# Kernel tuning notes

Hardware: AMD Instinct MI355X
Metric: run time of the kernel (lower is better)

The kernel has to match this reference:

```python
import jax, jax.numpy as jnp
import numpy as np

C = 128
N0, N1, N2 = 1000000, 100000, 10000


def setup_inputs() -> dict:
    key = jax.random.key(0)
    ks = jax.random.split(key, 9)
    return {
        "x0": jax.random.normal(ks[0], (N0, C), dtype=jnp.float32),
        "x1": jax.random.normal(ks[1], (N1, C), dtype=jnp.float32),
        "x2": jax.random.normal(ks[2], (N2, C), dtype=jnp.float32),
        "cluster1": jax.random.randint(ks[3], (N0,), 0, N1, dtype=jnp.int32),
        "cluster2": jax.random.randint(ks[4], (N1,), 0, N2, dtype=jnp.int32),
        "Wf2c0": jax.random.normal(ks[5], (C, C), dtype=jnp.float32) / np.sqrt(C),
        "Wf2c1": jax.random.normal(ks[6], (C, C), dtype=jnp.float32) / np.sqrt(C),
        "Wc2f0": jax.random.normal(ks[7], (C, C), dtype=jnp.float32) / np.sqrt(C),
        "Wc2f1": jax.random.normal(ks[8], (C, C), dtype=jnp.float32) / np.sqrt(C),
    }


def _segment_mean(x, idx, num_segments):
    # scatter-mean: sum per cluster / count (count clamped to 1 -> empty clusters give 0)
    s = jax.ops.segment_sum(x, idx, num_segments=num_segments)
    cnt = jax.ops.segment_sum(jnp.ones((x.shape[0], 1), x.dtype), idx, num_segments=num_segments)
    return s / jnp.maximum(cnt, 1.0)


def reference(x0, x1, x2, cluster1, cluster2, Wf2c0, Wf2c1, Wc2f0, Wc2f1):
    n1, n2 = x1.shape[0], x2.shape[0]
    # scale 0: x0 + gather(coarse_to_fine_0(x1), cluster1)
    y0 = x0 + (x1 @ Wc2f0.T)[cluster1]
    # scale 1: x1 + fine_to_coarse_0(scatter_mean(x0, cluster1)) + gather(coarse_to_fine_1(x2), cluster2)
    y1 = x1 + _segment_mean(x0, cluster1, n1) @ Wf2c0.T + (x2 @ Wc2f1.T)[cluster2]
    # scale 2: x2 + fine_to_coarse_1(scatter_mean(x1, cluster2))
    y2 = x2 + _segment_mean(x1, cluster2, n2) @ Wf2c1.T
    return (y0, y1, y2)
```

## Files before the change

kernel.cpp:

```cpp
#include <hip/hip_runtime.h>

#define C128 128
#define WSTRIDE 136

typedef __attribute__((ext_vector_type(2))) float f32x2;
typedef __attribute__((ext_vector_type(4))) float f32x4;
typedef __attribute__((ext_vector_type(8))) short short8;

__device__ __forceinline__ short f2bf(float f) {
  union { float f; unsigned u; } v; v.f = f;
  unsigned r = (v.u + 0x7fffu + ((v.u >> 16) & 1u)) >> 16;
  return (short)r;
}

__device__ __forceinline__ void stage_W(const float* __restrict__ W, ushort* Wl) {
  const int tid = threadIdx.x;
#pragma unroll
  for (int c = 0; c < 16; ++c) {
    const int e = (c * 256 + tid) * 4;
    const int row = e >> 7, col = e & 127;
    f32x4 v = *(const f32x4*)(W + e);
    ushort4 u;
    u.x = (ushort)f2bf(v.x); u.y = (ushort)f2bf(v.y);
    u.z = (ushort)f2bf(v.z); u.w = (ushort)f2bf(v.w);
    *(ushort4*)(Wl + row * WSTRIDE + col) = u;
  }
}

__device__ __forceinline__ void gemm_body(
    const float* __restrict__ A, const ushort* __restrict__ Wl,
    const float* __restrict__ add,
    const int* __restrict__ gidx, const float* __restrict__ gtab,
    float* __restrict__ out, int R, int blockrow)
{
  const int tid  = threadIdx.x;
  const int wave = tid >> 6;
  const int lane = tid & 63;
  const int r16  = lane & 15;
  const int kg   = lane >> 4;

  const int rowbase = blockrow + wave * 16;
  if (rowbase >= R) return;
  const int arow_i  = rowbase + r16;
  const int lrow    = arow_i < R ? arow_i : (R - 1);

  f32x4 acc[8];
#pragma unroll
  for (int i = 0; i < 8; ++i) acc[i] = (f32x4){0.f, 0.f, 0.f, 0.f};

  const float* arow = A + (long long)lrow * C128;

#pragma unroll
  for (int ks = 0; ks < 4; ++ks) {
    const int k0 = ks * 32 + kg * 8;
    f32x4 alo = *(const f32x4*)(arow + k0);
    f32x4 ahi = *(const f32x4*)(arow + k0 + 4);
    short8 af;
    af[0] = f2bf(alo.x); af[1] = f2bf(alo.y);
    af[2] = f2bf(alo.z); af[3] = f2bf(alo.w);
    af[4] = f2bf(ahi.x); af[5] = f2bf(ahi.y);
    af[6] = f2bf(ahi.z); af[7] = f2bf(ahi.w);
#pragma unroll
    for (int nf = 0; nf < 8; ++nf) {
      short8 bf = *(const short8*)(Wl + (nf * 16 + r16) * WSTRIDE + k0);
      acc[nf] = __builtin_amdgcn_mfma_f32_16x16x32_bf16(af, bf, acc[nf], 0, 0, 0);
    }
  }

#pragma unroll
  for (int i = 0; i < 4; ++i) {
    const int orow = rowbase + kg * 4 + i;
    if (orow >= R) continue;
    const float* addrow = add ? add + (long long)orow * C128 : nullptr;
    const float* grow = gidx ? gtab + (long long)gidx[orow] * C128 : nullptr;
    float* orow_p = out + (long long)orow * C128;
#pragma unroll
    for (int nf = 0; nf < 8; ++nf) {
      const int oc = nf * 16 + r16;
      float v = acc[nf][i];
      if (addrow) v += addrow[oc];
      if (grow)   v += grow[oc];
      orow_p[oc] = v;
    }
  }
}

__global__ __launch_bounds__(256) void pre_gemm(
    const float* __restrict__ x1, const float* __restrict__ W1, float* __restrict__ t1, int n1,
    const float* __restrict__ x2, const float* __restrict__ W2, float* __restrict__ t2, int n2,
    int* __restrict__ zbuf, int zlen, int B1)
{
  __shared__ ushort Wl[C128 * WSTRIDE];
  {
    const int nb  = gridDim.x;
    const int per = (zlen + nb - 1) / nb;
    const int zs  = blockIdx.x * per;
    const int ze  = (zs + per < zlen) ? zs + per : zlen;
    for (int k = zs + threadIdx.x; k < ze; k += 256) zbuf[k] = 0;
  }
  if ((int)blockIdx.x < B1) {
    stage_W(W1, Wl); __syncthreads();
    gemm_body(x1, Wl, nullptr, nullptr, nullptr, t1, n1, blockIdx.x * 64);
  } else {
    stage_W(W2, Wl); __syncthreads();
    gemm_body(x2, Wl, nullptr, nullptr, nullptr, t2, n2, (blockIdx.x - B1) * 64);
  }
}

__global__ __launch_bounds__(256) void post_gemm(
    const float* __restrict__ mean0, const float* __restrict__ Wa,
    const float* __restrict__ x1, const int* __restrict__ cluster2,
    const float* __restrict__ t2, float* __restrict__ y1, int n1,
    const float* __restrict__ mean1, const float* __restrict__ Wb,
    const float* __restrict__ x2, float* __restrict__ y2, int n2, int B1)
{
  __shared__ ushort Wl[C128 * WSTRIDE];
  if ((int)blockIdx.x < B1) {
    stage_W(Wa, Wl); __syncthreads();
    gemm_body(mean0, Wl, x1, cluster2, t2, y1, n1, blockIdx.x * 64);
  } else {
    stage_W(Wb, Wl); __syncthreads();
    gemm_body(mean1, Wl, x2, nullptr, nullptr, y2, n2, (blockIdx.x - B1) * 64);
  }
}

__global__ __launch_bounds__(256) void hist2(
    const int* __restrict__ cl1, int n0, int* __restrict__ cnt0,
    const int* __restrict__ cl2, int n1, int* __restrict__ cnt1)
{
  int i = blockIdx.x * blockDim.x + threadIdx.x;
  const int stride = gridDim.x * blockDim.x;
  const int total = n0 + n1;
  for (; i < total; i += stride) {
    if (i < n0) atomicAdd(&cnt0[cl1[i]], 1);
    else        atomicAdd(&cnt1[cl2[i - n0]], 1);
  }
}

__global__ __launch_bounds__(256) void scan2(
    const int* __restrict__ cnt0, int* __restrict__ off0, int* __restrict__ cur0, int n1,
    const int* __restrict__ cnt1, int* __restrict__ off1, int* __restrict__ cur1, int n2,
    int* __restrict__ tot)
{
  const int p1 = (n1 + 255) & ~255;
  const int i  = blockIdx.x * blockDim.x + threadIdx.x;
  const int lane = threadIdx.x & 63;

  const int* cnt; int* off; int* cur; int* t; int j; int nn;
  if (i < p1) { cnt = cnt0; off = off0; cur = cur0; t = tot + 0; j = i;      nn = n1; }
  else        { cnt = cnt1; off = off1; cur = cur1; t = tot + 1; j = i - p1; nn = n2; }

  int c = (j < nn) ? cnt[j] : 0;
  int pref = c;
#pragma unroll
  for (int d = 1; d < 64; d <<= 1) {
    int v = __shfl_up(pref, d);
    if (lane >= d) pref += v;
  }
  const int wave_total = __shfl(pref, 63);
  int base = 0;
  if (lane == 63) base = atomicAdd(t, wave_total);
  base = __shfl(base, 63);

  if (j < nn) {
    const int o = base + (pref - c);
    off[j] = o;
    cur[j] = o;
  }
}

__global__ __launch_bounds__(256) void fill2(
    const int* __restrict__ cl1, int n0, int* __restrict__ cur0, int* __restrict__ idx0,
    const int* __restrict__ cl2, int n1, int* __restrict__ cur1, int* __restrict__ idx1)
{
  int i = blockIdx.x * blockDim.x + threadIdx.x;
  const int stride = gridDim.x * blockDim.x;
  const int total = n0 + n1;
  for (; i < total; i += stride) {
    if (i < n0) { int p = atomicAdd(&cur0[cl1[i]], 1); idx0[p] = i; }
    else        { int k = i - n0; int p = atomicAdd(&cur1[cl2[k]], 1); idx1[p] = k; }
  }
}

__device__ __forceinline__ void cr_one(
    int wid, int lane, const float* __restrict__ x,
    const int* __restrict__ idxp, const int* __restrict__ offp,
    const int* __restrict__ cntp, const float* __restrict__ trow,
    float* __restrict__ yb, float* __restrict__ meanp)
{
  const int n = cntp[wid];
  const int o = offp[wid];

  f32x2 tc = {0.f, 0.f};
  if (trow) tc = ((const f32x2*)trow)[lane];

  f32x2 s0 = {0.f,0.f}, s1 = {0.f,0.f}, s2 = {0.f,0.f}, s3 = {0.f,0.f};
  for (int base = 0; base < n; base += 64) {
    int m = n - base; if (m > 64) m = 64;
    int vi = (lane < m) ? idxp[o + base + lane] : 0;
    int j = 0;
    for (; j + 3 < m; j += 4) {
      const long long i0 = __shfl(vi, j);
      const long long i1 = __shfl(vi, j + 1);
      const long long i2 = __shfl(vi, j + 2);
      const long long i3 = __shfl(vi, j + 3);
      f32x2 a = ((const f32x2*)(x + i0 * C128))[lane];
      f32x2 b = ((const f32x2*)(x + i1 * C128))[lane];
      f32x2 c = ((const f32x2*)(x + i2 * C128))[lane];
      f32x2 d = ((const f32x2*)(x + i3 * C128))[lane];
      s0 += a; s1 += b; s2 += c; s3 += d;
      if (yb) {
        ((f32x2*)(yb + i0 * C128))[lane] = a + tc;
        ((f32x2*)(yb + i1 * C128))[lane] = b + tc;
        ((f32x2*)(yb + i2 * C128))[lane] = c + tc;
        ((f32x2*)(yb + i3 * C128))[lane] = d + tc;
      }
    }
    for (; j < m; ++j) {
      const long long i0 = __shfl(vi, j);
      f32x2 a = ((const f32x2*)(x + i0 * C128))[lane];
      s0 += a;
      if (yb) ((f32x2*)(yb + i0 * C128))[lane] = a + tc;
    }
  }

  const float invn = n > 0 ? 1.0f / (float)n : 0.0f;
  ((f32x2*)(meanp + (long long)wid * C128))[lane] = ((s0 + s1) + (s2 + s3)) * invn;
}

__global__ __launch_bounds__(256) void cluster_reduce2(
    const float* __restrict__ x0, const int* __restrict__ idx0,
    const int* __restrict__ off0, const int* __restrict__ cnt0,
    const float* __restrict__ t1, float* __restrict__ y0,
    float* __restrict__ mean0, int n1,
    const float* __restrict__ x1, const int* __restrict__ idx1,
    const int* __restrict__ off1, const int* __restrict__ cnt1,
    float* __restrict__ mean1, int n2)
{
  const int wid  = blockIdx.x * 4 + (threadIdx.x >> 6);
  const int lane = threadIdx.x & 63;
  if (wid >= n1 + n2) return;

  if (wid < n1)
    cr_one(wid, lane, x0, idx0, off0, cnt0,
           t1 + (long long)wid * C128, y0, mean0);
  else
    cr_one(wid - n1, lane, x1, idx1, off1, cnt1,
           nullptr, nullptr, mean1);
}

extern "C" void kernel_launch(void* const* d_in, const int* in_sizes, int n_in,
                              void* d_out, int out_size, void* d_ws, size_t ws_size,
                              hipStream_t stream)
{
  const float* x0 = (const float*)d_in[0];
  const float* x1 = (const float*)d_in[1];
  const float* x2 = (const float*)d_in[2];
  const int* cluster1 = (const int*)d_in[3];
  const int* cluster2 = (const int*)d_in[4];
  const float* Wf2c0 = (const float*)d_in[5];
  const float* Wf2c1 = (const float*)d_in[6];
  const float* Wc2f0 = (const float*)d_in[7];
  const float* Wc2f1 = (const float*)d_in[8];

  const int N0 = in_sizes[0] / C128;
  const int N1 = in_sizes[1] / C128;
  const int N2 = in_sizes[2] / C128;

  float* y0 = (float*)d_out;
  float* y1 = y0 + (long long)N0 * C128;
  float* y2 = y1 + (long long)N1 * C128;

  float* mean0 = y1;
  float* mean1 = y2;

  float* t1 = (float*)d_ws;
  float* t2 = t1 + (long long)N1 * C128;
  int* cnt0 = (int*)(t2 + (long long)N2 * C128);
  int* cnt1 = cnt0 + N1;
  int* tot  = cnt1 + N2;
  int* off0 = tot + 2;
  int* off1 = off0 + N1;
  int* cur0 = off1 + N2;
  int* cur1 = cur0 + N1;
  int* idx0 = cur1 + N2;
  int* idx1 = idx0 + N0;

  const int B1 = (N1 + 63) / 64;
  const int B2 = (N2 + 63) / 64;

  pre_gemm<<<B1 + B2, 256, 0, stream>>>(
      x1, Wc2f0, t1, N1, x2, Wc2f1, t2, N2, cnt0, N1 + N2 + 2, B1);

  int bh = (N0 + N1 + 255) / 256; if (bh > 2048) bh = 2048;
  hist2<<<bh, 256, 0, stream>>>(cluster1, N0, cnt0, cluster2, N1, cnt1);
  const int p1 = (N1 + 255) & ~255, p2 = (N2 + 255) & ~255;
  scan2<<<(p1 + p2) / 256, 256, 0, stream>>>(
      cnt0, off0, cur0, N1, cnt1, off1, cur1, N2, tot);
  fill2<<<bh, 256, 0, stream>>>(cluster1, N0, cur0, idx0, cluster2, N1, cur1, idx1);

  cluster_reduce2<<<(N1 + N2 + 3) / 4, 256, 0, stream>>>(
      x0, idx0, off0, cnt0, t1, y0, mean0, N1,
      x1, idx1, off1, cnt1, mean1, N2);

  post_gemm<<<B1 + B2, 256, 0, stream>>>(
      mean0, Wf2c0, x1, cluster2, t2, y1, N1,
      mean1, Wf2c1, x2, y2, N2, B1);
}
```

Before: 502.1 us.

## Pre-convert weights to bf16 once and fuse histogram into pre-GEMM kernel

Adds a small prep kernel that zeroes the count buffers and converts all four weight matrices to bf16 in workspace once, instead of every GEMM block staging and converting W into LDS. GEMM kernels now read bf16 B fragments straight from global memory (via cache) and drop the LDS tile and barrier. The histogram atomics are folded into the pre-GEMM kernel, removing one launch. The trade-off is that B fragments are re-read from L2 by every wave, and the atomics now share blocks with the GEMM work.

Result: no change. 499.3 us (-0.6%).

```diff
diff --git a/kernel.cpp b/kernel.cpp
--- a/kernel.cpp
+++ b/kernel.cpp
@@ -1,7 +1,6 @@
 #include <hip/hip_runtime.h>
 
 #define C128 128
-#define WSTRIDE 136
 
 typedef __attribute__((ext_vector_type(2))) float f32x2;
 typedef __attribute__((ext_vector_type(4))) float f32x4;
@@ -13,22 +12,22 @@
   return (short)r;
 }
 
-__device__ __forceinline__ void stage_W(const float* __restrict__ W, ushort* Wl) {
-  const int tid = threadIdx.x;
-#pragma unroll
-  for (int c = 0; c < 16; ++c) {
-    const int e = (c * 256 + tid) * 4;
-    const int row = e >> 7, col = e & 127;
-    f32x4 v = *(const f32x4*)(W + e);
-    ushort4 u;
-    u.x = (ushort)f2bf(v.x); u.y = (ushort)f2bf(v.y);
-    u.z = (ushort)f2bf(v.z); u.w = (ushort)f2bf(v.w);
-    *(ushort4*)(Wl + row * WSTRIDE + col) = u;
+__global__ __launch_bounds__(256) void prep(
+    const float* __restrict__ Wa, const float* __restrict__ Wb_,
+    const float* __restrict__ Wc, const float* __restrict__ Wd,
+    ushort* __restrict__ Wout, int* __restrict__ zbuf, int zlen)
+{
+  const int tid = blockIdx.x * 256 + threadIdx.x;
+  const int nth = gridDim.x * 256;
+  for (int k = tid; k < zlen; k += nth) zbuf[k] = 0;
+  for (int k = tid; k < 4 * 16384; k += nth) {
+    const float* W = (k < 16384) ? Wa : (k < 32768) ? Wb_ : (k < 49152) ? Wc : Wd;
+    Wout[k] = (ushort)f2bf(W[k & 16383]);
   }
 }
 
 __device__ __forceinline__ void gemm_body(
-    const float* __restrict__ A, const ushort* __restrict__ Wl,
+    const float* __restrict__ A, const ushort* __restrict__ Wb,
     const float* __restrict__ add,
     const int* __restrict__ gidx, const float* __restrict__ gtab,
     float* __restrict__ out, int R, int blockrow)
@@ -62,7 +61,7 @@
     af[6] = f2bf(ahi.z); af[7] = f2bf(ahi.w);
 #pragma unroll
     for (int nf = 0; nf < 8; ++nf) {
-      short8 bf = *(const short8*)(Wl + (nf * 16 + r16) * WSTRIDE + k0);
+      short8 bf = *(const short8*)(Wb + (nf * 16 + r16) * C128 + k0);
       acc[nf] = __builtin_amdgcn_mfma_f32_16x16x32_bf16(af, bf, acc[nf], 0, 0, 0);
     }
   }
@@ -85,56 +84,38 @@
   }
 }
 
-__global__ __launch_bounds__(256) void pre_gemm(
-    const float* __restrict__ x1, const float* __restrict__ W1, float* __restrict__ t1, int n1,
-    const float* __restrict__ x2, const float* __restrict__ W2, float* __restrict__ t2, int n2,
-    int* __restrict__ zbuf, int zlen, int B1)
-{
-  __shared__ ushort Wl[C128 * WSTRIDE];
+__global__ __launch_bounds__(256) void pre_hist_gemm(
+    const float* __restrict__ x1, const ushort* __restrict__ W1b, float* __restrict__ t1, int n1,
+    const float* __restrict__ x2, const ushort* __restrict__ W2b, float* __restrict__ t2, int n2,
+    const int* __restrict__ cl1, int n0, int* __restrict__ cnt0,
+    const int* __restrict__ cl2, int* __restrict__ cnt1, int B1)
+{
   {
-    const int nb  = gridDim.x;
-    const int per = (zlen + nb - 1) / nb;
-    const int zs  = blockIdx.x * per;
-    const int ze  = (zs + per < zlen) ? zs + per : zlen;
-    for (int k = zs + threadIdx.x; k < ze; k += 256) zbuf[k] = 0;
-  }
-  if ((int)blockIdx.x < B1) {
-    stage_W(W1, Wl); __syncthreads();
-    gemm_body(x1, Wl, nullptr, nullptr, nullptr, t1, n1, blockIdx.x * 64);
-  } else {
-    stage_W(W2, Wl); __syncthreads();
-    gemm_body(x2, Wl, nullptr, nullptr, nullptr, t2, n2, (blockIdx.x - B1) * 64);
-  }
+    int i = blockIdx.x * 256 + threadIdx.x;
+    const int nth = gridDim.x * 256;
+    const int total = n0 + n1;
+    for (; i < total; i += nth) {
+      if (i < n0) atomicAdd(&cnt0[cl1[i]], 1);
+      else        atomicAdd(&cnt1[cl2[i - n0]], 1);
+    }
+  }
+  if ((int)blockIdx.x < B1)
+    gemm_body(x1, W1b, nullptr, nullptr, nullptr, t1, n1, blockIdx.x * 64);
+  else
+    gemm_body(x2, W2b, nullptr, nullptr, nullptr, t2, n2, (blockIdx.x - B1) * 64);
 }
 
 __global__ __launch_bounds__(256) void post_gemm(
-    const float* __restrict__ mean0, const float* __restrict__ Wa,
+    const float* __restrict__ mean0, const ushort* __restrict__ Wab,
     const float* __restrict__ x1, const int* __restrict__ cluster2,
     const float* __restrict__ t2, float* __restrict__ y1, int n1,
-    const float* __restrict__ mean1, const float* __restrict__ Wb,
+    const float* __restrict__ mean1, const ushort* __restrict__ Wbb,
     const float* __restrict__ x2, float* __restrict__ y2, int n2, int B1)
 {
-  __shared__ ushort Wl[C128 * WSTRIDE];
-  if ((int)blockIdx.x < B1) {
-    stage_W(Wa, Wl); __syncthreads();
-    gemm_body(mean0, Wl, x1, cluster2, t2, y1, n1, blockIdx.x * 64);
-  } else {
-    stage_W(Wb, Wl); __syncthreads();
-    gemm_body(mean1, Wl, x2, nullptr, nullptr, y2, n2, (blockIdx.x - B1) * 64);
-  }
-}
-
-__global__ __launch_bounds__(256) void hist2(
-    const int* __restrict__ cl1, int n0, int* __restrict__ cnt0,
-    const int* __restrict__ cl2, int n1, int* __restrict__ cnt1)
-{
-  int i = blockIdx.x * blockDim.x + threadIdx.x;
-  const int stride = gridDim.x * blockDim.x;
-  const int total = n0 + n1;
-  for (; i < total; i += stride) {
-    if (i < n0) atomicAdd(&cnt0[cl1[i]], 1);
-    else        atomicAdd(&cnt1[cl2[i - n0]], 1);
-  }
+  if ((int)blockIdx.x < B1)
+    gemm_body(mean0, Wab, x1, cluster2, t2, y1, n1, blockIdx.x * 64);
+  else
+    gemm_body(mean1, Wbb, x2, nullptr, nullptr, y2, n2, (blockIdx.x - B1) * 64);
 }
 
 __global__ __launch_bounds__(256) void scan2(
@@ -285,18 +266,26 @@
   int* cur1 = cur0 + N1;
   int* idx0 = cur1 + N2;
   int* idx1 = idx0 + N0;
+  ushort* Wb = (ushort*)(idx1 + N1);
+  ushort* Wb_c2f0 = Wb;
+  ushort* Wb_c2f1 = Wb + 16384;
+  ushort* Wb_f2c0 = Wb + 32768;
+  ushort* Wb_f2c1 = Wb + 49152;
 
   const int B1 = (N1 + 63) / 64;
   const int B2 = (N2 + 63) / 64;
 
-  pre_gemm<<<B1 + B2, 256, 0, stream>>>(
-      x1, Wc2f0, t1, N1, x2, Wc2f1, t2, N2, cnt0, N1 + N2 + 2, B1);
-
-  int bh = (N0 + N1 + 255) / 256; if (bh > 2048) bh = 2048;
-  hist2<<<bh, 256, 0, stream>>>(cluster1, N0, cnt0, cluster2, N1, cnt1);
+  prep<<<256, 256, 0, stream>>>(
+      Wc2f0, Wc2f1, Wf2c0, Wf2c1, Wb, cnt0, N1 + N2 + 2);
+
+  pre_hist_gemm<<<B1 + B2, 256, 0, stream>>>(
+      x1, Wb_c2f0, t1, N1, x2, Wb_c2f1, t2, N2,
+      cluster1, N0, cnt0, cluster2, cnt1, B1);
+
   const int p1 = (N1 + 255) & ~255, p2 = (N2 + 255) & ~255;
   scan2<<<(p1 + p2) / 256, 256, 0, stream>>>(
       cnt0, off0, cur0, N1, cnt1, off1, cur1, N2, tot);
+  int bh = (N0 + N1 + 255) / 256; if (bh > 2048) bh = 2048;
   fill2<<<bh, 256, 0, stream>>>(cluster1, N0, cur0, idx0, cluster2, N1, cur1, idx1);
 
   cluster_reduce2<<<(N1 + N2 + 3) / 4, 256, 0, stream>>>(
@@ -304,6 +293,6 @@
       x1, idx1, off1, cnt1, mean1, N2);
 
   post_gemm<<<B1 + B2, 256, 0, stream>>>(
-      mean0, Wf2c0, x1, cluster2, t2, y1, N1,
-      mean1, Wf2c1, x2, y2, N2, B1);
-}
+      mean0, Wb_f2c0, x1, cluster2, t2, y1, N1,
+      mean1, Wb_f2c1, x2, y2, N2, B1);
+}
```
